# Optimization experiments

Hardware: AMD Instinct MI355X
Metric: run time of the kernel (lower is better)

## Reference

```python
import jax, jax.numpy as jnp
import numpy as np

D_MODEL, NHEAD, D_FF, N_EXP, TOP_K = 1024, 16, 4096, 8, 2
EPS = 1e-5


def setup_inputs() -> dict:
    key = jax.random.key(0)
    ks = jax.random.split(key, 16)
    s = 0.02
    B, S, d = 4, 1024, D_MODEL
    return {
        'src': jax.random.normal(ks[0], (B, S, d), jnp.float32),
        'in_proj_w': jax.random.normal(ks[1], (3 * d, d), jnp.float32) * s,
        'in_proj_b': jnp.zeros((3 * d,), jnp.float32),
        'out_proj_w': jax.random.normal(ks[2], (d, d), jnp.float32) * s,
        'out_proj_b': jnp.zeros((d,), jnp.float32),
        'ln1_g': jnp.ones((d,), jnp.float32),
        'ln1_b': jnp.zeros((d,), jnp.float32),
        'router_w': jax.random.normal(ks[3], (N_EXP, d), jnp.float32) * s,
        'router_b': jnp.zeros((N_EXP,), jnp.float32),
        'w1': jax.random.normal(ks[4], (N_EXP, d, D_FF), jnp.float32) * s,
        'b1': jnp.zeros((N_EXP, D_FF), jnp.float32),
        'w2': jax.random.normal(ks[5], (N_EXP, D_FF, d), jnp.float32) * s,
        'b2': jnp.zeros((N_EXP, d), jnp.float32),
        'ln2_g': jnp.ones((d,), jnp.float32),
        'ln2_b': jnp.zeros((d,), jnp.float32),
    }


def layer_norm(x, g, b):
    mu = x.mean(-1, keepdims=True)
    var = ((x - mu) ** 2).mean(-1, keepdims=True)
    return (x - mu) * jax.lax.rsqrt(var + EPS) * g + b


def mha(x, wqkv, bqkv, wo, bo):
    B, S, d = x.shape
    dh = d // NHEAD
    qkv = x @ wqkv.T + bqkv                      # [B,S,3d]
    q, k, v = jnp.split(qkv, 3, axis=-1)
    def heads(t):
        return t.reshape(B, S, NHEAD, dh).transpose(0, 2, 1, 3)  # [B,h,S,dh]
    q, k, v = heads(q), heads(k), heads(v)
    scores = jnp.einsum('bhqd,bhkd->bhqk', q, k) / jnp.sqrt(jnp.float32(dh))
    a = jax.nn.softmax(scores, axis=-1)
    o = jnp.einsum('bhqk,bhkd->bhqd', a, v)
    o = o.transpose(0, 2, 1, 3).reshape(B, S, d)
    return o @ wo.T + bo


def moe(x, router_w, router_b, w1, b1, w2, b2):
    B, S, d = x.shape
    xt = x.reshape(-1, d)                         # [T,d]
    logits = xt @ router_w.T + router_b           # [T,E]
    probs = jax.nn.softmax(logits, axis=-1)
    topv, topi = jax.lax.top_k(probs, TOP_K)      # [T,k]
    mask = jax.nn.one_hot(topi, N_EXP, dtype=xt.dtype).sum(1)  # [T,E] 0/1
    gates = probs * mask
    gates = gates / gates.sum(-1, keepdims=True)  # renormalized top-k weights
    # dense expert compute, weighted combine (zero gate => no contribution)
    h = jax.nn.relu(jnp.einsum('td,edf->etf', xt, w1) + b1[:, None, :])
    y = jnp.einsum('etf,efd->etd', h, w2) + b2[:, None, :]
    out = jnp.einsum('te,etd->td', gates, y).reshape(B, S, d)
    # Switch-style load balancing loss
    f = mask.mean(0) / TOP_K                      # fraction of assignments
    P = probs.mean(0)                             # mean router prob
    lb = jnp.float32(N_EXP) * jnp.sum(f * P)
    return out, lb


def reference(src, in_proj_w, in_proj_b, out_proj_w, out_proj_b, ln1_g, ln1_b,
              router_w, router_b, w1, b1, w2, b2, ln2_g, ln2_b):
    a = mha(src, in_proj_w, in_proj_b, out_proj_w, out_proj_b)
    x = layer_norm(src + a, ln1_g, ln1_b)
    m, lb = moe(x, router_w, router_b, w1, b1, w2, b2)
    x = layer_norm(x + m, ln2_g, ln2_b)
    return x, lb
```

## Files before the change

### kernel.cpp

```cpp
#include <hip/hip_runtime.h>


typedef __attribute__((ext_vector_type(8))) short short8;
typedef __attribute__((ext_vector_type(4))) short short4v;
typedef __attribute__((ext_vector_type(4))) float floatx4;

#define TOKENS 4096
#define DMODEL 1024
#define NHEADS 16
#define DHEAD  64
#define DFF    4096
#define NEXP   8
#define SEQ    1024
#define NPAIR  64

__device__ inline short f2bf(float f) {
  unsigned u = __builtin_bit_cast(unsigned, f);
  unsigned r = (u + 0x7fffu + ((u >> 16) & 1u)) >> 16;
  return (short)r;
}
__device__ inline float bf2f(short h) {
  return __builtin_bit_cast(float, ((unsigned)(unsigned short)h) << 16);
}

__device__ inline void gload16(const short* g, short* l) {
  __builtin_amdgcn_global_load_lds(
      (const __attribute__((address_space(1))) unsigned int*)g,
      (__attribute__((address_space(3))) unsigned int*)l, 16, 0, 0);
}

template<int BM, int BN, int WTM, int WTN, int EPI, int AMODE, bool RELU, bool SPLIT>
__global__ void __launch_bounds__((BM / WTM) * (BN / WTN) * 64)
gemm_nt(const short* __restrict__ Ab, const short* __restrict__ Abl, int lda, long sA,
        const short* __restrict__ Bb, const short* __restrict__ Bbl, int ldb, long sB,
        void* __restrict__ Cb, int ldc, long sC,
        int M, int N, int K, float scale,
        const float* __restrict__ bias, int sBias,
        const float* __restrict__ srcadd,
        const int* __restrict__ tokList,
        const int* __restrict__ counts,
        const int* __restrict__ offsets)
{
  constexpr int WROWS = BM / WTM;
  constexpr int WCOLS = BN / WTN;
  constexpr int NW = WROWS * WCOLS;
  constexpr int MT = WTM / 16;
  constexpr int NT = WTN / 16;
  constexpr int ISSA = (BM / 16) / NW;
  constexpr int ISSB = (BN / 16) / NW;
  constexpr int PL = SPLIT ? 2 : 1;
  constexpr int ABUF = PL * BM * 32;
  constexpr int BBUF = PL * BN * 32;

  int xw, yw, zw;
  if (AMODE != 0) {
    int flat = blockIdx.x + gridDim.x * (blockIdx.y + gridDim.y * blockIdx.z);
    zw = flat & 7;
    int m = flat >> 3;
    xw = m % gridDim.x;
    yw = m / gridDim.x;
  } else {
    int nwg = gridDim.x * gridDim.y;
    int f2 = blockIdx.x + gridDim.x * blockIdx.y;
    int cpx = nwg >> 3;
    int g = (f2 & 7) * cpx + (f2 >> 3);
    xw = g % gridDim.x;
    yw = g / gridDim.x;
    zw = blockIdx.z;
  }

  const int z = zw;
  int Mt = M;
  int rowbase = 0;
  const int* tl = nullptr;
  if (AMODE != 0) {
    Mt = counts[z];
    if (xw * BM >= Mt) return;
    if (AMODE == 1) tl = tokList + offsets[z];
    else rowbase = offsets[z];
  }

  const short* A = Ab + (long)z * sA;
  const short* Al = SPLIT ? (Abl + (long)z * sA) : nullptr;
  const short* B = Bb + (long)z * sB;
  const short* Bl = SPLIT ? (Bbl + (long)z * sB) : nullptr;
  const int tid = threadIdx.x;
  const int lane = tid & 63;
  const int w = tid >> 6;
  const int wrow = w % WROWS;
  const int wcol = w / WROWS;
  const int m0 = xw * BM;
  const int n0 = yw * BN;

  __shared__ __align__(16) short As[2 * ABUF];
  __shared__ __align__(16) short Bs[2 * BBUF];

  const int l4 = lane >> 2;
  const int lc = (lane & 3) ^ (l4 & 3) ^ ((lane >> 4) & 3);
  long agp[ISSA]; int albase[ISSA];
#pragma unroll
  for (int r = 0; r < ISSA; ++r) {
    int seg = w * ISSA + r;
    int row = seg * 16 + l4;
    int grow;
    if (AMODE == 0) grow = m0 + row;
    else if (AMODE == 1) grow = tl[min(m0 + row, Mt - 1)];
    else grow = rowbase + min(m0 + row, Mt - 1);
    agp[r] = (long)grow * lda + lc * 8;
    albase[r] = seg * 512;
  }
  long bgp[ISSB]; int blbase[ISSB];
#pragma unroll
  for (int r = 0; r < ISSB; ++r) {
    int seg = w * ISSB + r;
    int row = seg * 16 + l4;
    bgp[r] = (long)(n0 + row) * ldb + lc * 8;
    blbase[r] = seg * 512;
  }

  floatx4 acc[MT][NT];
#pragma unroll
  for (int i = 0; i < MT; ++i)
#pragma unroll
    for (int j = 0; j < NT; ++j) acc[i][j] = floatx4{0.f, 0.f, 0.f, 0.f};

  const int am = wrow * WTM + (lane & 15);
  const int bn = wcol * WTN + (lane & 15);
  const int ac = lane >> 4;
  const int aro = am * 32 + ((ac ^ (am & 3) ^ ((am >> 2) & 3)) << 3);
  const int bro = bn * 32 + ((ac ^ (bn & 3) ^ ((bn >> 2) & 3)) << 3);

  auto stage = [&](int buf, int k0) {
    short* Ad = &As[buf * ABUF];
    short* Bd = &Bs[buf * BBUF];
#pragma unroll
    for (int r = 0; r < ISSA; ++r) gload16(A + agp[r] + k0, Ad + albase[r]);
#pragma unroll
    for (int r = 0; r < ISSB; ++r) gload16(B + bgp[r] + k0, Bd + blbase[r]);
    if (SPLIT) {
#pragma unroll
      for (int r = 0; r < ISSA; ++r) gload16(Al + agp[r] + k0, Ad + BM * 32 + albase[r]);
#pragma unroll
      for (int r = 0; r < ISSB; ++r) gload16(Bl + bgp[r] + k0, Bd + BN * 32 + blbase[r]);
    }
  };

  auto compute = [&](int buf) {
    const short* Ar = &As[buf * ABUF];
    const short* Br = &Bs[buf * BBUF];
    short8 afh[MT], bfh[NT];
#pragma unroll
    for (int i = 0; i < MT; ++i) afh[i] = *(const short8*)&Ar[aro + i * 512];
#pragma unroll
    for (int j = 0; j < NT; ++j) bfh[j] = *(const short8*)&Br[bro + j * 512];
    if (SPLIT) {
      short8 afl[MT], bfl[NT];
#pragma unroll
      for (int i = 0; i < MT; ++i) afl[i] = *(const short8*)&Ar[BM * 32 + aro + i * 512];
#pragma unroll
      for (int j = 0; j < NT; ++j) bfl[j] = *(const short8*)&Br[BN * 32 + bro + j * 512];
#pragma unroll
      for (int i = 0; i < MT; ++i)
#pragma unroll
        for (int j = 0; j < NT; ++j) {
          acc[i][j] = __builtin_amdgcn_mfma_f32_16x16x32_bf16(afh[i], bfh[j], acc[i][j], 0, 0, 0);
          acc[i][j] = __builtin_amdgcn_mfma_f32_16x16x32_bf16(afh[i], bfl[j], acc[i][j], 0, 0, 0);
          acc[i][j] = __builtin_amdgcn_mfma_f32_16x16x32_bf16(afl[i], bfh[j], acc[i][j], 0, 0, 0);
        }
    } else {
#pragma unroll
      for (int i = 0; i < MT; ++i)
#pragma unroll
        for (int j = 0; j < NT; ++j)
          acc[i][j] = __builtin_amdgcn_mfma_f32_16x16x32_bf16(afh[i], bfh[j], acc[i][j], 0, 0, 0);
    }
  };

  const int ntile = K >> 5;
  stage(0, 0);
  __syncthreads();
  int cur = 0;
  for (int t = 0; t < ntile - 1; ++t) {
    compute(cur);
    stage(cur ^ 1, (t + 1) << 5);
    __syncthreads();
    cur ^= 1;
  }
  compute(cur);

  const float* bz = bias ? (bias + (long)z * sBias) : nullptr;
#pragma unroll
  for (int i = 0; i < MT; ++i) {
    int rt = wrow * WTM + i * 16 + ((lane >> 4) << 2);
#pragma unroll
    for (int j = 0; j < NT; ++j) {
      int col = n0 + wcol * WTN + j * 16 + (lane & 15);
      float badd = bz ? bz[col] : 0.f;
      floatx4 v = acc[i][j];
#pragma unroll
      for (int q = 0; q < 4; ++q) {
        int r = m0 + rt + q;
        if (AMODE != 0 && r >= Mt) break;
        long orow = (AMODE == 1) ? ((long)offsets[z] + r)
                  : (AMODE == 2) ? ((long)rowbase + r) : (long)r;
        float val = v[q] * scale + badd;
        if (RELU) val = fmaxf(val, 0.f);
        if (EPI == 0) {
          ((short*)Cb)[(long)z * sC + orow * ldc + col] = f2bf(val);
        } else {
          float* Cf = (float*)Cb + (long)z * sC;
          if (srcadd) val += srcadd[orow * ldc + col];
          Cf[orow * ldc + col] = val;
        }
      }
    }
  }
}

__global__ void split_bf16(const float* __restrict__ src, short* __restrict__ hi,
                           short* __restrict__ lo, int n) {
  int i = (blockIdx.x * 256 + threadIdx.x) * 4;
  if (i >= n) return;
  float4 v = *(const float4*)(src + i);
  short h0 = f2bf(v.x), h1 = f2bf(v.y), h2 = f2bf(v.z), h3 = f2bf(v.w);
  short4v oh = { h0, h1, h2, h3 };
  short4v ol = { f2bf(v.x - bf2f(h0)), f2bf(v.y - bf2f(h1)),
                 f2bf(v.z - bf2f(h2)), f2bf(v.w - bf2f(h3)) };
  *(short4v*)(hi + i) = oh;
  *(short4v*)(lo + i) = ol;
}

__global__ void transpose_bf16(const float* __restrict__ src, short* __restrict__ dst,
                               int R, int C) {
  __shared__ float t[64][65];
  long zoff = (long)blockIdx.z * R * C;
  const float* s = src + zoff;
  short* d = dst + zoff;
  int r0 = blockIdx.y * 64, c0 = blockIdx.x * 64;
  int tid = threadIdx.x;
#pragma unroll
  for (int i = 0; i < 16; ++i) {
    int flat = i * 256 + tid;
    int r = flat >> 6, c = flat & 63;
    t[r][c] = s[(long)(r0 + r) * C + c0 + c];
  }
  __syncthreads();
#pragma unroll
  for (int i = 0; i < 16; ++i) {
    int flat = i * 256 + tid;
    int c = flat >> 6, r = flat & 63;
    d[(long)(c0 + c) * R + r0 + r] = f2bf(t[r][c]);
  }
}

__global__ void repack_qkv_split(const float* __restrict__ qkv,
                                 short* __restrict__ Qh, short* __restrict__ Ql,
                                 short* __restrict__ Kh, short* __restrict__ Kl,
                                 short* __restrict__ Vh, short* __restrict__ Vl) {
  long idx = (long)blockIdx.x * 256 + threadIdx.x;
  int t = (int)(idx / 3072), c = (int)(idx % 3072);
  int sec = c >> 10, within = c & 1023;
  int h = within >> 6, di = within & 63;
  int b = t >> 10, s = t & 1023;
  int g = b * NHEADS + h;
  float v = qkv[idx];
  short vh = f2bf(v);
  short vl = f2bf(v - bf2f(vh));
  if (sec == 2) {
    long vo = (long)g * 65536 + di * 1024 + s;
    Vh[vo] = vh; Vl[vo] = vl;
  } else {
    long qo = (long)g * 65536 + s * 64 + di;
    if (sec == 0) { Qh[qo] = vh; Ql[qo] = vl; }
    else          { Kh[qo] = vh; Kl[qo] = vl; }
  }
}

__global__ void softmax_rows_split(float* __restrict__ scores) {
  __shared__ float wred[4], wsum[4];
  long row = blockIdx.x;
  float* p = scores + row * 1024;
  int tid = threadIdx.x;
  float4 v = *(const float4*)(p + tid * 4);
  float mx = fmaxf(fmaxf(v.x, v.y), fmaxf(v.z, v.w));
  for (int m = 1; m < 64; m <<= 1) mx = fmaxf(mx, __shfl_xor(mx, m));
  if ((tid & 63) == 0) wred[tid >> 6] = mx;
  __syncthreads();
  mx = fmaxf(fmaxf(wred[0], wred[1]), fmaxf(wred[2], wred[3]));
  float e0 = expf(v.x - mx), e1 = expf(v.y - mx), e2 = expf(v.z - mx), e3 = expf(v.w - mx);
  float sm = e0 + e1 + e2 + e3;
  for (int m = 1; m < 64; m <<= 1) sm += __shfl_xor(sm, m);
  if ((tid & 63) == 0) wsum[tid >> 6] = sm;
  __syncthreads();
  float inv = 1.f / (wsum[0] + wsum[1] + wsum[2] + wsum[3]);
  float y0 = e0 * inv, y1 = e1 * inv, y2 = e2 * inv, y3 = e3 * inv;
  short h0 = f2bf(y0), h1 = f2bf(y1), h2 = f2bf(y2), h3 = f2bf(y3);
  short4v oh = { h0, h1, h2, h3 };
  short4v ol = { f2bf(y0 - bf2f(h0)), f2bf(y1 - bf2f(h1)),
                 f2bf(y2 - bf2f(h2)), f2bf(y3 - bf2f(h3)) };
  short* ps = (short*)p;
  *(short4v*)(ps + tid * 4) = oh;
  *(short4v*)(ps + 1024 + tid * 4) = ol;
}

__global__ void ln_rows(const float* __restrict__ x, const float* __restrict__ g,
                        const float* __restrict__ b, float* __restrict__ of,
                        short* __restrict__ ob) {
  __shared__ float ws1[4], ws2[4];
  long row = blockIdx.x;
  const float* p = x + row * 1024;
  int tid = threadIdx.x;
  float4 v = *(const float4*)(p + tid * 4);
  float s = v.x + v.y + v.z + v.w;
  float s2 = v.x * v.x + v.y * v.y + v.z * v.z + v.w * v.w;
  for (int m = 1; m < 64; m <<= 1) { s += __shfl_xor(s, m); s2 += __shfl_xor(s2, m); }
  if ((tid & 63) == 0) { ws1[tid >> 6] = s; ws2[tid >> 6] = s2; }
  __syncthreads();
  s = ws1[0] + ws1[1] + ws1[2] + ws1[3];
  s2 = ws2[0] + ws2[1] + ws2[2] + ws2[3];
  float mean = s * (1.f / 1024.f);
  float var = s2 * (1.f / 1024.f) - mean * mean;
  float rstd = rsqrtf(var + 1e-5f);
  float4 gg = *(const float4*)(g + tid * 4);
  float4 bb = *(const float4*)(b + tid * 4);
  float y0 = (v.x - mean) * rstd * gg.x + bb.x;
  float y1 = (v.y - mean) * rstd * gg.y + bb.y;
  float y2 = (v.z - mean) * rstd * gg.z + bb.z;
  float y3 = (v.w - mean) * rstd * gg.w + bb.w;
  if (of) { float4 o = { y0, y1, y2, y3 }; *(float4*)(of + row * 1024 + tid * 4) = o; }
  if (ob) { short4v o = { f2bf(y0), f2bf(y1), f2bf(y2), f2bf(y3) }; *(short4v*)(ob + row * 1024 + tid * 4) = o; }
}

__global__ void combine_ln2(const float* __restrict__ accum, const float* __restrict__ y,
                            const int* __restrict__ pos1, const int* __restrict__ pos2,
                            const float* __restrict__ g1a, const float* __restrict__ g2a,
                            const float* __restrict__ gn, const float* __restrict__ bn,
                            float* __restrict__ out) {
  __shared__ float ws1[4], ws2[4];
  int t = blockIdx.x;
  int tid = threadIdx.x;
  const float* a = accum + (long)t * 1024;
  const float* y1 = y + (long)pos1[t] * 1024;
  const float* y2 = y + (long)pos2[t] * 1024;
  float G1 = g1a[t], G2 = g2a[t];
  float4 va = *(const float4*)(a + tid * 4);
  float4 v1 = *(const float4*)(y1 + tid * 4);
  float4 v2 = *(const float4*)(y2 + tid * 4);
  float x0 = va.x + G1 * v1.x + G2 * v2.x;
  float x1 = va.y + G1 * v1.y + G2 * v2.y;
  float x2 = va.z + G1 * v1.z + G2 * v2.z;
  float x3 = va.w + G1 * v1.w + G2 * v2.w;
  float s = x0 + x1 + x2 + x3;
  float s2 = x0 * x0 + x1 * x1 + x2 * x2 + x3 * x3;
  for (int m = 1; m < 64; m <<= 1) { s += __shfl_xor(s, m); s2 += __shfl_xor(s2, m); }
  if ((tid & 63) == 0) { ws1[tid >> 6] = s; ws2[tid >> 6] = s2; }
  __syncthreads();
  s = ws1[0] + ws1[1] + ws1[2] + ws1[3];
  s2 = ws2[0] + ws2[1] + ws2[2] + ws2[3];
  float mean = s * (1.f / 1024.f);
  float var = s2 * (1.f / 1024.f) - mean * mean;
  float rstd = rsqrtf(var + 1e-5f);
  float4 gg = *(const float4*)(gn + tid * 4);
  float4 bb = *(const float4*)(bn + tid * 4);
  float4 o = { (x0 - mean) * rstd * gg.x + bb.x,
               (x1 - mean) * rstd * gg.y + bb.y,
               (x2 - mean) * rstd * gg.z + bb.z,
               (x3 - mean) * rstd * gg.w + bb.w };
  *(float4*)(out + (long)t * 1024 + tid * 4) = o;
}

__global__ void router_compute(const float* __restrict__ x, const float* __restrict__ rw,
                               const float* __restrict__ rb,
                               int* __restrict__ top1, int* __restrict__ top2,
                               float* __restrict__ g1o, float* __restrict__ g2o,
                               float* __restrict__ partialP) {
  __shared__ float pp[4][8];
  int w = threadIdx.x >> 6, lane = threadIdx.x & 63;
  int t = blockIdx.x * 4 + w;
  const float* xp = x + (long)t * 1024;
  float xv[16];
#pragma unroll
  for (int i = 0; i < 16; ++i) xv[i] = xp[lane + i * 64];
  float logit[8];
#pragma unroll
  for (int e = 0; e < 8; ++e) {
    const float* wp = rw + e * 1024;
    double a = 0.0;
#pragma unroll
    for (int i = 0; i < 16; ++i) a += (double)xv[i] * (double)wp[lane + i * 64];
    for (int m = 1; m < 64; m <<= 1) a += __shfl_xor(a, m);
    logit[e] = (float)a + rb[e];
  }
  float mx = logit[0];
#pragma unroll
  for (int e = 1; e < 8; ++e) mx = fmaxf(mx, logit[e]);
  float pe[8], sum = 0.f;
#pragma unroll
  for (int e = 0; e < 8; ++e) { pe[e] = expf(logit[e] - mx); sum += pe[e]; }
  float inv = 1.f / sum;
#pragma unroll
  for (int e = 0; e < 8; ++e) pe[e] *= inv;
  int i1 = 0;
#pragma unroll
  for (int e = 1; e < 8; ++e) if (pe[e] > pe[i1]) i1 = e;
  int i2 = (i1 == 0) ? 1 : 0;
#pragma unroll
  for (int e = 0; e < 8; ++e) if (e != i1 && pe[e] > pe[i2]) i2 = e;
  float denom = pe[i1] + pe[i2];
  if (lane == 0) {
    top1[t] = i1; top2[t] = i2;
    g1o[t] = pe[i1] / denom; g2o[t] = pe[i2] / denom;
#pragma unroll
    for (int e = 0; e < 8; ++e) pp[w][e] = pe[e];
  }
  __syncthreads();
  if (threadIdx.x < 8) {
    partialP[(long)blockIdx.x * 8 + threadIdx.x] =
        pp[0][threadIdx.x] + pp[1][threadIdx.x] + pp[2][threadIdx.x] + pp[3][threadIdx.x];
  }
}

__global__ void __launch_bounds__(1024) router_finalize(
    const float* __restrict__ partialP,
    const int* __restrict__ top1, const int* __restrict__ top2,
    int* __restrict__ counts, int* __restrict__ eoff_out,
    int* __restrict__ tokList, int* __restrict__ pos1, int* __restrict__ pos2,
    float* __restrict__ lb_out) {
  __shared__ float redP[16][8];
  __shared__ int wtot[16][8];
  __shared__ int tot[8], eoff[8];
  __shared__ float psum[8];
  int tid = threadIdx.x;
  int lane = tid & 63, wv = tid >> 6;

  float p[8];
#pragma unroll
  for (int e = 0; e < 8; ++e) p[e] = partialP[(long)tid * 8 + e];
  for (int m = 1; m < 64; m <<= 1)
#pragma unroll
    for (int e = 0; e < 8; ++e) p[e] += __shfl_xor(p[e], m);
  if (lane == 0)
#pragma unroll
    for (int e = 0; e < 8; ++e) redP[wv][e] = p[e];

  int c[8] = {0, 0, 0, 0, 0, 0, 0, 0};
  int expid[8];
#pragma unroll
  for (int j = 0; j < 8; ++j) {
    int i = tid * 8 + j;
    int t = i >> 1;
    int e = (i & 1) ? top2[t] : top1[t];
    expid[j] = e;
    c[e]++;
  }
  int inc[8];
#pragma unroll
  for (int e = 0; e < 8; ++e) inc[e] = c[e];
  for (int d = 1; d < 64; d <<= 1) {
#pragma unroll
    for (int e = 0; e < 8; ++e) {
      int o = __shfl_up(inc[e], d);
      if (lane >= d) inc[e] += o;
    }
  }
  if (lane == 63)
#pragma unroll
    for (int e = 0; e < 8; ++e) wtot[wv][e] = inc[e];
  __syncthreads();
  if (tid < 8) {
    int run = 0;
#pragma unroll
    for (int w = 0; w < 16; ++w) { int v = wtot[w][tid]; wtot[w][tid] = run; run += v; }
    tot[tid] = run;
    float s = 0.f;
#pragma unroll
    for (int w = 0; w < 16; ++w) s += redP[w][tid];
    psum[tid] = s;
  }
  __syncthreads();
  if (tid == 0) {
    int off = 0;
#pragma unroll
    for (int e = 0; e < 8; ++e) { eoff[e] = off; off += tot[e]; }
  }
  __syncthreads();
  int base[8], c2[8] = {0, 0, 0, 0, 0, 0, 0, 0};
#pragma unroll
  for (int e = 0; e < 8; ++e) base[e] = eoff[e] + wtot[wv][e] + inc[e] - c[e];
#pragma unroll
  for (int j = 0; j < 8; ++j) {
    int i = tid * 8 + j;
    int t = i >> 1;
    int e = expid[j];
    int dest = base[e] + c2[e]++;
    tokList[dest] = t;
    if (i & 1) pos2[t] = dest; else pos1[t] = dest;
  }
  if (tid < 8) { counts[tid] = tot[tid]; eoff_out[tid] = eoff[tid]; }
  if (tid == 0) {
    float lb = 0.f;
#pragma unroll
    for (int e = 0; e < 8; ++e)
      lb += ((float)tot[e] / 8192.f) * (psum[e] / 4096.f);
    *lb_out = 8.f * lb;
  }
}

__global__ void sentinel_kernel(float* out, int n) {
  if (threadIdx.x == 0) { out[0] = 1e9f; out[n - 1] = 1e9f; }
}

extern "C" void kernel_launch(void* const* d_in, const int* in_sizes, int n_in,
                              void* d_out, int out_size, void* d_ws, size_t ws_size,
                              hipStream_t stream) {
  const float* src        = (const float*)d_in[0];
  const float* in_proj_w  = (const float*)d_in[1];
  const float* in_proj_b  = (const float*)d_in[2];
  const float* out_proj_w = (const float*)d_in[3];
  const float* out_proj_b = (const float*)d_in[4];
  const float* ln1_g      = (const float*)d_in[5];
  const float* ln1_b      = (const float*)d_in[6];
  const float* router_w   = (const float*)d_in[7];
  const float* router_b   = (const float*)d_in[8];
  const float* w1         = (const float*)d_in[9];
  const float* b1         = (const float*)d_in[10];
  const float* w2         = (const float*)d_in[11];
  const float* b2         = (const float*)d_in[12];
  const float* ln2_g      = (const float*)d_in[13];
  const float* ln2_b      = (const float*)d_in[14];
  float* out = (float*)d_out;

  char* ws = (char*)d_ws;
  size_t off = 0;
  auto alloc = [&](size_t bytes) -> char* {
    char* p = ws + off;
    off += (bytes + 255) & ~(size_t)255;
    return p;
  };
  char*  blockW = alloc(8ll * (DFF * DMODEL + DMODEL * DFF) * 2);
  short* Qh = (short*)(blockW + 0ll  * 1024 * 1024);
  short* Ql = (short*)(blockW + 8ll  * 1024 * 1024);
  short* Kh = (short*)(blockW + 16ll * 1024 * 1024);
  short* Kl = (short*)(blockW + 24ll * 1024 * 1024);
  short* Vh = (short*)(blockW + 32ll * 1024 * 1024);
  short* Vl = (short*)(blockW + 40ll * 1024 * 1024);
  short* w1t = (short*)blockW;
  short* w2t = (short*)(blockW + 8ll * DFF * DMODEL * 2);
  short* winh  = (short*)alloc(3072ll * 1024 * 2);
  short* winl  = (short*)alloc(3072ll * 1024 * 2);
  short* wouth = (short*)alloc(1024ll * 1024 * 2);
  short* woutl = (short*)alloc(1024ll * 1024 * 2);
  short* xh    = (short*)alloc((long)TOKENS * DMODEL * 2);
  short* xl    = (short*)alloc((long)TOKENS * DMODEL * 2);
  char*  reg1  = alloc((long)TOKENS * 3072 * 4);
  float* qkvf  = (float*)reg1;
  float* Of32  = (float*)reg1;
  short* Ohi   = (short*)(reg1 + 16ll * 1024 * 1024);
  short* Olo   = (short*)(reg1 + 24ll * 1024 * 1024);
  float* x1    = (float*)(reg1 + 32ll * 1024 * 1024);
  float* y     = (float*)reg1;
  char*  reg2  = alloc(16ll * 1024 * 1024 * 4);
  float* scores = (float*)reg2;
  short* h      = (short*)reg2;
  short* x1nbf = (short*)alloc((long)TOKENS * DMODEL * 2);
  float* accum = (float*)alloc((long)TOKENS * DMODEL * 4);
  float* partialP = (float*)alloc(1024 * 8 * 4);
  int*   top1   = (int*)alloc(TOKENS * 4);
  int*   top2   = (int*)alloc(TOKENS * 4);
  float* g1a    = (float*)alloc(TOKENS * 4);
  float* g2a    = (float*)alloc(TOKENS * 4);
  int*   pos1   = (int*)alloc(TOKENS * 4);
  int*   pos2   = (int*)alloc(TOKENS * 4);
  int*   counts = (int*)alloc(32);
  int*   eoff   = (int*)alloc(32);
  int*   tokList = (int*)alloc(2 * TOKENS * 4);
  size_t needed = off;

  if (ws_size < needed) {
    sentinel_kernel<<<1, 64, 0, stream>>>(out, out_size);
    return;
  }

  split_bf16<<<3072 * 1024 / 1024, 256, 0, stream>>>(in_proj_w, winh, winl, 3072 * 1024);
  split_bf16<<<1024 * 1024 / 1024, 256, 0, stream>>>(out_proj_w, wouth, woutl, 1024 * 1024);
  split_bf16<<<TOKENS * DMODEL / 1024, 256, 0, stream>>>(src, xh, xl, TOKENS * DMODEL);

  gemm_nt<128, 128, 64, 64, 1, 0, false, true><<<dim3(32, 24, 1), 256, 0, stream>>>(
      xh, xl, 1024, 0, winh, winl, 1024, 0, qkvf, 3072, 0,
      TOKENS, 3072, 1024, 1.f, in_proj_b, 0, nullptr, nullptr, nullptr, nullptr);
  repack_qkv_split<<<(int)((long)TOKENS * 3072 / 256), 256, 0, stream>>>(qkvf, Qh, Ql, Kh, Kl, Vh, Vl);

  for (int c = 0; c < 4; ++c) {
    long co = (long)c * 16 * 65536;
    gemm_nt<128, 128, 64, 64, 1, 0, false, true><<<dim3(8, 8, 16), 256, 0, stream>>>(
        Qh + co, Ql + co, 64, 65536, Kh + co, Kl + co, 64, 65536, scores, 1024, 1048576,
        1024, 1024, 64, 0.125f, nullptr, 0, nullptr, nullptr, nullptr, nullptr);
    softmax_rows_split<<<16 * 1024, 256, 0, stream>>>(scores);
    gemm_nt<128, 64, 64, 32, 1, 0, false, true><<<dim3(8, 1, 16), 256, 0, stream>>>(
        (const short*)scores, (const short*)scores + 1024, 2048, 2097152,
        Vh + co, Vl + co, 1024, 65536,
        Of32 + (long)c * 1048576, 1024, 64,
        1024, 64, 1024, 1.f, nullptr, 0, nullptr, nullptr, nullptr, nullptr);
  }

  transpose_bf16<<<dim3(DFF / 64, DMODEL / 64, 8), 256, 0, stream>>>(w1, w1t, DMODEL, DFF);
  transpose_bf16<<<dim3(DMODEL / 64, DFF / 64, 8), 256, 0, stream>>>(w2, w2t, DFF, DMODEL);

  split_bf16<<<TOKENS * DMODEL / 1024, 256, 0, stream>>>(Of32, Ohi, Olo, TOKENS * DMODEL);
  gemm_nt<128, 128, 64, 64, 1, 0, false, true><<<dim3(32, 8, 1), 256, 0, stream>>>(
      Ohi, Olo, 1024, 0, wouth, woutl, 1024, 0, x1, 1024, 0,
      TOKENS, 1024, 1024, 1.f, out_proj_b, 0, src, nullptr, nullptr, nullptr);

  ln_rows<<<TOKENS, 256, 0, stream>>>(x1, ln1_g, ln1_b, accum, x1nbf);

  router_compute<<<TOKENS / 4, 256, 0, stream>>>(accum, router_w, router_b,
                                                 top1, top2, g1a, g2a, partialP);
  router_finalize<<<1, 1024, 0, stream>>>(partialP, top1, top2, counts, eoff,
                                          tokList, pos1, pos2, out + (out_size - 1));

  gemm_nt<128, 128, 64, 64, 0, 1, true, false><<<dim3(32, 32, 8), 256, 0, stream>>>(
      x1nbf, nullptr, 1024, 0, w1t, nullptr, 1024, (long)DFF * DMODEL, h, DFF, 0,
      0, DFF, 1024, 1.f, b1, DFF, nullptr, tokList, counts, eoff);

  gemm_nt<128, 128, 64, 64, 1, 2, false, false><<<dim3(32, 8, 8), 256, 0, stream>>>(
      h, nullptr, DFF, 0, w2t, nullptr, DFF, (long)DMODEL * DFF, y, 1024, 0,
      0, DMODEL, DFF, 1.f, b2, DMODEL, nullptr, tokList, counts, eoff);

  combine_ln2<<<TOKENS, 256, 0, stream>>>(accum, y, pos1, pos2, g1a, g2a,
                                          ln2_g, ln2_b, out);
}
```

Before: 1.164 ms.

## Fuse attention into a single flash-style kernel with online softmax

Replaces the per-chunk QK^T GEMM, row softmax and PV GEMM (plus the split of the fp32 output) with one fused kernel. It streams K/V tiles through shared memory, keeps an online-softmax running max and sum in registers, and writes the bf16 hi/lo output directly. This removes the round trips of the 16M-entry score matrix through global memory and several launches. The cost is more register pressure and a per-tile rescaling step, and only 512 blocks do sequential work across 16 KV tiles.

```diff
diff --git a/kernel.cpp b/kernel.cpp
--- a/kernel.cpp
+++ b/kernel.cpp
@@ -217,6 +217,185 @@
   }
 }
 
+__global__ void __launch_bounds__(256)
+fused_attn(const short* __restrict__ Qh, const short* __restrict__ Ql,
+           const short* __restrict__ Kh, const short* __restrict__ Kl,
+           const short* __restrict__ Vh, const short* __restrict__ Vl,
+           short* __restrict__ Ohi, short* __restrict__ Olo)
+{
+  const int f = blockIdx.x + 8 * blockIdx.z;
+  const int pair = (f & 7) + ((f >> 6) << 3);
+  const int qt = (f >> 3) & 7;
+  const long pb = (long)pair * 65536;
+  const int lane = threadIdx.x & 63;
+  const int w = threadIdx.x >> 6;
+  const int qb0 = qt * 128;
+
+  __shared__ __align__(16) short Ksh[4096], Ksl[4096];
+  __shared__ __align__(16) short Vsh[4096], Vsl[4096];
+  __shared__ __align__(16) short Ph[4][32 * 72], Pl[4][32 * 72];
+
+  short8 qfh[2][2], qfl[2][2];
+#pragma unroll
+  for (int i = 0; i < 2; ++i)
+#pragma unroll
+    for (int kt = 0; kt < 2; ++kt) {
+      long qoff = pb + (long)(qb0 + w * 32 + i * 16 + (lane & 15)) * 64
+                + (lane >> 4) * 8 + kt * 32;
+      qfh[i][kt] = *(const short8*)&Qh[qoff];
+      qfl[i][kt] = *(const short8*)&Ql[qoff];
+    }
+
+  floatx4 oacc[2][4];
+#pragma unroll
+  for (int i = 0; i < 2; ++i)
+#pragma unroll
+    for (int jd = 0; jd < 4; ++jd) oacc[i][jd] = floatx4{0.f, 0.f, 0.f, 0.f};
+  float mrow[2][4], lrow[2][4];
+#pragma unroll
+  for (int i = 0; i < 2; ++i)
+#pragma unroll
+    for (int q = 0; q < 4; ++q) { mrow[i][q] = -1e30f; lrow[i][q] = 0.f; }
+
+  const int r8 = lane >> 3, pc8 = lane & 7;
+  const int lc8 = ((pc8 ^ r8) & 7) * 8;
+
+  for (int t = 0; t < 16; ++t) {
+    const int kv0 = t * 64;
+    __syncthreads();
+#pragma unroll
+    for (int s = 0; s < 2; ++s) {
+      int seg = w * 2 + s;
+      long krow = kv0 + seg * 8 + r8;
+      gload16(&Kh[pb + krow * 64 + lc8], &Ksh[seg * 512]);
+      gload16(&Kl[pb + krow * 64 + lc8], &Ksl[seg * 512]);
+      long drow = seg * 8 + r8;
+      gload16(&Vh[pb + drow * 1024 + kv0 + lc8], &Vsh[seg * 512]);
+      gload16(&Vl[pb + drow * 1024 + kv0 + lc8], &Vsl[seg * 512]);
+    }
+    __syncthreads();
+
+    floatx4 sacc[2][4];
+#pragma unroll
+    for (int i = 0; i < 2; ++i)
+#pragma unroll
+      for (int j = 0; j < 4; ++j) sacc[i][j] = floatx4{0.f, 0.f, 0.f, 0.f};
+#pragma unroll
+    for (int j = 0; j < 4; ++j) {
+      int rr = j * 16 + (lane & 15);
+      int base = rr * 64, rsw = rr & 7;
+#pragma unroll
+      for (int kt = 0; kt < 2; ++kt) {
+        int kc = (lane >> 4) + kt * 4;
+        int off = base + ((kc ^ rsw) << 3);
+        short8 kh8 = *(const short8*)&Ksh[off];
+        short8 kl8 = *(const short8*)&Ksl[off];
+#pragma unroll
+        for (int i = 0; i < 2; ++i) {
+          sacc[i][j] = __builtin_amdgcn_mfma_f32_16x16x32_bf16(qfh[i][kt], kh8, sacc[i][j], 0, 0, 0);
+          sacc[i][j] = __builtin_amdgcn_mfma_f32_16x16x32_bf16(qfh[i][kt], kl8, sacc[i][j], 0, 0, 0);
+          sacc[i][j] = __builtin_amdgcn_mfma_f32_16x16x32_bf16(qfl[i][kt], kh8, sacc[i][j], 0, 0, 0);
+        }
+      }
+    }
+#pragma unroll
+    for (int i = 0; i < 2; ++i)
+#pragma unroll
+      for (int j = 0; j < 4; ++j) sacc[i][j] *= 0.125f;
+
+#pragma unroll
+    for (int i = 0; i < 2; ++i)
+#pragma unroll
+      for (int q = 0; q < 4; ++q) {
+        float tm = fmaxf(fmaxf(sacc[i][0][q], sacc[i][1][q]),
+                         fmaxf(sacc[i][2][q], sacc[i][3][q]));
+#pragma unroll
+        for (int msk = 1; msk < 16; msk <<= 1) tm = fmaxf(tm, __shfl_xor(tm, msk));
+        float mold = mrow[i][q];
+        float mn = fmaxf(mold, tm);
+        float c = expf(mold - mn);
+        mrow[i][q] = mn;
+        float ts = 0.f;
+#pragma unroll
+        for (int j = 0; j < 4; ++j) {
+          float p = expf(sacc[i][j][q] - mn);
+          sacc[i][j][q] = p;
+          ts += p;
+        }
+#pragma unroll
+        for (int msk = 1; msk < 16; msk <<= 1) ts += __shfl_xor(ts, msk);
+        lrow[i][q] = lrow[i][q] * c + ts;
+#pragma unroll
+        for (int jd = 0; jd < 4; ++jd) oacc[i][jd][q] *= c;
+      }
+
+    short* php = Ph[w];
+    short* plp = Pl[w];
+#pragma unroll
+    for (int i = 0; i < 2; ++i)
+#pragma unroll
+      for (int j = 0; j < 4; ++j)
+#pragma unroll
+        for (int q = 0; q < 4; ++q) {
+          float p = sacc[i][j][q];
+          short ph_ = f2bf(p);
+          short pl_ = f2bf(p - bf2f(ph_));
+          int row = i * 16 + ((lane >> 4) << 2) + q;
+          int col = j * 16 + (lane & 15);
+          php[row * 72 + col] = ph_;
+          plp[row * 72 + col] = pl_;
+        }
+    asm volatile("s_waitcnt lgkmcnt(0)" ::: "memory");
+    __builtin_amdgcn_sched_barrier(0);
+
+    short8 pah[2][2], pal[2][2];
+#pragma unroll
+    for (int i = 0; i < 2; ++i)
+#pragma unroll
+      for (int kt = 0; kt < 2; ++kt) {
+        int off = (i * 16 + (lane & 15)) * 72 + (lane >> 4) * 8 + kt * 32;
+        pah[i][kt] = *(const short8*)&php[off];
+        pal[i][kt] = *(const short8*)&plp[off];
+      }
+#pragma unroll
+    for (int jd = 0; jd < 4; ++jd) {
+      int rr = jd * 16 + (lane & 15);
+      int base = rr * 64, rsw = rr & 7;
+#pragma unroll
+      for (int kt = 0; kt < 2; ++kt) {
+        int kc = (lane >> 4) + kt * 4;
+        int off = base + ((kc ^ rsw) << 3);
+        short8 vh8 = *(const short8*)&Vsh[off];
+        short8 vl8 = *(const short8*)&Vsl[off];
+#pragma unroll
+        for (int i = 0; i < 2; ++i) {
+          oacc[i][jd] = __builtin_amdgcn_mfma_f32_16x16x32_bf16(pah[i][kt], vh8, oacc[i][jd], 0, 0, 0);
+          oacc[i][jd] = __builtin_amdgcn_mfma_f32_16x16x32_bf16(pah[i][kt], vl8, oacc[i][jd], 0, 0, 0);
+          oacc[i][jd] = __builtin_amdgcn_mfma_f32_16x16x32_bf16(pal[i][kt], vh8, oacc[i][jd], 0, 0, 0);
+        }
+      }
+    }
+  }
+
+  const int b = pair >> 4, hh = pair & 15;
+#pragma unroll
+  for (int i = 0; i < 2; ++i)
+#pragma unroll
+    for (int q = 0; q < 4; ++q) {
+      float inv = 1.f / lrow[i][q];
+      int qrow = qb0 + w * 32 + i * 16 + ((lane >> 4) << 2) + q;
+      long obase = (long)(b * 1024 + qrow) * 1024 + hh * 64;
+#pragma unroll
+      for (int jd = 0; jd < 4; ++jd) {
+        float v = oacc[i][jd][q] * inv;
+        short vh_ = f2bf(v);
+        long oi = obase + jd * 16 + (lane & 15);
+        Ohi[oi] = vh_;
+        Olo[oi] = f2bf(v - bf2f(vh_));
+      }
+    }
+}
+
 __global__ void split_bf16(const float* __restrict__ src, short* __restrict__ hi,
                            short* __restrict__ lo, int n) {
   int i = (blockIdx.x * 256 + threadIdx.x) * 4;
@@ -274,33 +453,6 @@
     if (sec == 0) { Qh[qo] = vh; Ql[qo] = vl; }
     else          { Kh[qo] = vh; Kl[qo] = vl; }
   }
-}
-
-__global__ void softmax_rows_split(float* __restrict__ scores) {
-  __shared__ float wred[4], wsum[4];
-  long row = blockIdx.x;
-  float* p = scores + row * 1024;
-  int tid = threadIdx.x;
-  float4 v = *(const float4*)(p + tid * 4);
-  float mx = fmaxf(fmaxf(v.x, v.y), fmaxf(v.z, v.w));
-  for (int m = 1; m < 64; m <<= 1) mx = fmaxf(mx, __shfl_xor(mx, m));
-  if ((tid & 63) == 0) wred[tid >> 6] = mx;
-  __syncthreads();
-  mx = fmaxf(fmaxf(wred[0], wred[1]), fmaxf(wred[2], wred[3]));
-  float e0 = expf(v.x - mx), e1 = expf(v.y - mx), e2 = expf(v.z - mx), e3 = expf(v.w - mx);
-  float sm = e0 + e1 + e2 + e3;
-  for (int m = 1; m < 64; m <<= 1) sm += __shfl_xor(sm, m);
-  if ((tid & 63) == 0) wsum[tid >> 6] = sm;
-  __syncthreads();
-  float inv = 1.f / (wsum[0] + wsum[1] + wsum[2] + wsum[3]);
-  float y0 = e0 * inv, y1 = e1 * inv, y2 = e2 * inv, y3 = e3 * inv;
-  short h0 = f2bf(y0), h1 = f2bf(y1), h2 = f2bf(y2), h3 = f2bf(y3);
-  short4v oh = { h0, h1, h2, h3 };
-  short4v ol = { f2bf(y0 - bf2f(h0)), f2bf(y1 - bf2f(h1)),
-                 f2bf(y2 - bf2f(h2)), f2bf(y3 - bf2f(h3)) };
-  short* ps = (short*)p;
-  *(short4v*)(ps + tid * 4) = oh;
-  *(short4v*)(ps + 1024 + tid * 4) = ol;
 }
 
 __global__ void ln_rows(const float* __restrict__ x, const float* __restrict__ g,
@@ -554,13 +706,11 @@
   short* xl    = (short*)alloc((long)TOKENS * DMODEL * 2);
   char*  reg1  = alloc((long)TOKENS * 3072 * 4);
   float* qkvf  = (float*)reg1;
-  float* Of32  = (float*)reg1;
   short* Ohi   = (short*)(reg1 + 16ll * 1024 * 1024);
   short* Olo   = (short*)(reg1 + 24ll * 1024 * 1024);
   float* x1    = (float*)(reg1 + 32ll * 1024 * 1024);
   float* y     = (float*)reg1;
   char*  reg2  = alloc(16ll * 1024 * 1024 * 4);
-  float* scores = (float*)reg2;
   short* h      = (short*)reg2;
   short* x1nbf = (short*)alloc((long)TOKENS * DMODEL * 2);
   float* accum = (float*)alloc((long)TOKENS * DMODEL * 4);
@@ -590,23 +740,11 @@
       TOKENS, 3072, 1024, 1.f, in_proj_b, 0, nullptr, nullptr, nullptr, nullptr);
   repack_qkv_split<<<(int)((long)TOKENS * 3072 / 256), 256, 0, stream>>>(qkvf, Qh, Ql, Kh, Kl, Vh, Vl);
 
-  for (int c = 0; c < 4; ++c) {
-    long co = (long)c * 16 * 65536;
-    gemm_nt<128, 128, 64, 64, 1, 0, false, true><<<dim3(8, 8, 16), 256, 0, stream>>>(
-        Qh + co, Ql + co, 64, 65536, Kh + co, Kl + co, 64, 65536, scores, 1024, 1048576,
-        1024, 1024, 64, 0.125f, nullptr, 0, nullptr, nullptr, nullptr, nullptr);
-    softmax_rows_split<<<16 * 1024, 256, 0, stream>>>(scores);
-    gemm_nt<128, 64, 64, 32, 1, 0, false, true><<<dim3(8, 1, 16), 256, 0, stream>>>(
-        (const short*)scores, (const short*)scores + 1024, 2048, 2097152,
-        Vh + co, Vl + co, 1024, 65536,
-        Of32 + (long)c * 1048576, 1024, 64,
-        1024, 64, 1024, 1.f, nullptr, 0, nullptr, nullptr, nullptr, nullptr);
-  }
+  fused_attn<<<dim3(8, 1, 64), 256, 0, stream>>>(Qh, Ql, Kh, Kl, Vh, Vl, Ohi, Olo);
 
   transpose_bf16<<<dim3(DFF / 64, DMODEL / 64, 8), 256, 0, stream>>>(w1, w1t, DMODEL, DFF);
   transpose_bf16<<<dim3(DMODEL / 64, DFF / 64, 8), 256, 0, stream>>>(w2, w2t, DFF, DMODEL);
 
-  split_bf16<<<TOKENS * DMODEL / 1024, 256, 0, stream>>>(Of32, Ohi, Olo, TOKENS * DMODEL);
   gemm_nt<128, 128, 64, 64, 1, 0, false, true><<<dim3(32, 8, 1), 256, 0, stream>>>(
       Ohi, Olo, 1024, 0, wouth, woutl, 1024, 0, x1, 1024, 0,
       TOKENS, 1024, 1024, 1.f, out_proj_b, 0, src, nullptr, nullptr, nullptr);
```

After: 956.1 us. 1.22x faster.
